# Kernel optimization log

Hardware: AMD Instinct MI355X
Metric: run time of the kernel (lower is better)

The kernel has to match this reference:

```python
import jax, jax.numpy as jnp
import numpy as np

NUM_HEADS = 4
LN_EPS = 1e-5


def layer_norm(x, g, b):
    mu = jnp.mean(x, axis=-1, keepdims=True)
    var = jnp.mean(jnp.square(x - mu), axis=-1, keepdims=True)
    return (x - mu) * jax.lax.rsqrt(var + LN_EPS) * g + b


def setup_inputs() -> dict:
    key = jax.random.key(0)
    ks = jax.random.split(key, 18)
    N, E, D = 40000, 640000, 128
    H = 4 * D  # MLP hidden
    s = 0.02
    inp = {
        'node_features': jax.random.normal(ks[0], (N, D), jnp.float32),
        'edge_index': jax.random.randint(ks[1], (2, E), 0, N, jnp.int64),
        'Wq': jax.random.normal(ks[2], (D, D), jnp.float32) * s,
        'bq': jnp.zeros((D,), jnp.float32),
        'Wk': jax.random.normal(ks[3], (D, D), jnp.float32) * s,
        'bk': jnp.zeros((D,), jnp.float32),
        'Wv': jax.random.normal(ks[4], (D, D), jnp.float32) * s,
        'bv': jnp.zeros((D,), jnp.float32),
        'Wo': jax.random.normal(ks[5], (D, D), jnp.float32) * s,
        'bo': jnp.zeros((D,), jnp.float32),
        'ln_g': jnp.ones((D,), jnp.float32),
        'ln_b': jnp.zeros((D,), jnp.float32),
        'W1': jax.random.normal(ks[6], (D, H), jnp.float32) * s,
        'b1': jnp.zeros((H,), jnp.float32),
        'W2': jax.random.normal(ks[7], (H, D), jnp.float32) * s,
        'b2': jnp.zeros((D,), jnp.float32),
    }
    return inp


def reference(node_features, edge_index, Wq, bq, Wk, bk, Wv, bv, Wo, bo,
              ln_g, ln_b, W1, b1, W2, b2):
    N, D = node_features.shape
    Hh = NUM_HEADS
    hd = D // Hh
    residual = node_features

    q = (node_features @ Wq + bq).reshape(N, Hh, hd)
    k = (node_features @ Wk + bk).reshape(N, Hh, hd)
    v = (node_features @ Wv + bv).reshape(N, Hh, hd)

    src, dst = edge_index[0], edge_index[1]
    # per-edge attention scores: [E, Hh]
    scores = jnp.einsum('ehd,ehd->eh', q[dst], k[src]) * (hd ** -0.5)

    # segment softmax over edges grouped by destination node
    seg_max = jax.ops.segment_max(scores, dst, num_segments=N)  # [N, Hh]
    seg_max = jnp.where(jnp.isfinite(seg_max), seg_max, 0.0)
    ex = jnp.exp(scores - seg_max[dst])
    seg_sum = jax.ops.segment_sum(ex, dst, num_segments=N)  # [N, Hh]
    w = ex / seg_sum[dst]  # [E, Hh]

    messages = w[:, :, None] * v[src]  # [E, Hh, hd]
    aggregated = jax.ops.segment_sum(messages, dst, num_segments=N)  # [N, Hh, hd]
    aggregated = aggregated.reshape(N, D)

    out = aggregated @ Wo + bo
    out = layer_norm(out + residual, ln_g, ln_b)
    mlp = jax.nn.gelu(out @ W1 + b1) @ W2 + b2
    return out + mlp
```

## Files before the change

kernel.cpp:

```cpp
#include <hip/hip_runtime.h>
#include <math.h>

#define D   128
#define HH  4
#define HD  32
#define HID 512
#define WPB 4
#define MT  32
#define XP  136
#define HHP 264
#define KVB 264
#define SCB 1024

typedef __attribute__((ext_vector_type(8))) short bf16x8;
typedef __attribute__((ext_vector_type(4))) float f32x4;
typedef __attribute__((ext_vector_type(2))) float f32x2;

__device__ __forceinline__ short f2b(float f) {
    unsigned u = __float_as_uint(f);
    unsigned r = (u + 0x7FFFu + ((u >> 16) & 1u)) >> 16;
    return (short)r;
}
__device__ __forceinline__ unsigned char f2fp8(float f) {
    return (unsigned char)(__builtin_amdgcn_cvt_pk_fp8_f32(f, f, 0, false) & 0xFF);
}

__device__ __forceinline__ float gelu_tanh(float x) {
    float u = 0.7978845608028654f * (x + 0.044715f * x * x * x);
    float e = __expf(2.0f * u);
    return x * e * __builtin_amdgcn_rcpf(e + 1.0f);
}

__global__ void k0_zero_deg(int* __restrict__ deg, int N) {
    int i = blockIdx.x * blockDim.x + threadIdx.x;
    if (i < N) deg[i] = 0;
}

__global__ void k_prep(const float* __restrict__ W1, const float* __restrict__ W2,
                       const float* __restrict__ Wq, const float* __restrict__ Wk,
                       const float* __restrict__ Wv, const float* __restrict__ Wo,
                       short* __restrict__ Wt1, short* __restrict__ Wt2,
                       short* __restrict__ Wtq, short* __restrict__ Wtk,
                       short* __restrict__ Wtv, short* __restrict__ Wto) {
    int i = blockIdx.x * 256 + threadIdx.x;
    {   int n = i >> 7, k = i & 127; Wt1[i] = f2b(W1[k * HID + n]); }
    {   int n = i >> 9, k = i & 511; Wt2[i] = f2b(W2[k * D + n]); }
    if (i < D * D) {
        int n = i >> 7, k = i & 127;
        Wtq[i] = f2b(Wq[k * D + n]);
        Wtk[i] = f2b(Wk[k * D + n]);
        Wtv[i] = f2b(Wv[k * D + n]);
        Wto[i] = f2b(Wo[k * D + n]);
    }
}

__global__ __launch_bounds__(256) void k1_qkv_mfma(
        const float* __restrict__ x,
        const short* __restrict__ Wtq, const float* __restrict__ bq,
        const short* __restrict__ Wtk, const float* __restrict__ bk,
        const short* __restrict__ Wtv, const float* __restrict__ bv,
        float* __restrict__ q, unsigned char* __restrict__ kv, int N) {
    __shared__ short xs[MT * XP];
    __shared__ unsigned char kvs[MT * KVB];
    int m0 = blockIdx.x * MT;
    int t = threadIdx.x;
    int wave = t >> 6, lane = t & 63, quad = lane >> 4, l16 = lane & 15;

    {
        int row = t >> 3, c0 = (t & 7) * 16;
        int n = m0 + row;
        #pragma unroll
        for (int c = 0; c < 16; c += 4) {
            float4 xv = {0.f, 0.f, 0.f, 0.f};
            if (n < N) xv = *(const float4*)(x + (size_t)n * D + c0 + c);
            xs[row * XP + c0 + c + 0] = f2b(xv.x);
            xs[row * XP + c0 + c + 1] = f2b(xv.y);
            xs[row * XP + c0 + c + 2] = f2b(xv.z);
            xs[row * XP + c0 + c + 3] = f2b(xv.w);
        }
    }
    __syncthreads();

    f32x4 accq[2][2], acck[2][2], accv[2][2];
    #pragma unroll
    for (int nt = 0; nt < 2; ++nt) {
        int c = wave * 32 + nt * 16 + l16;
        float q0 = bq[c], k0 = bk[c], v0 = bv[c];
        #pragma unroll
        for (int mt = 0; mt < 2; ++mt) {
            accq[mt][nt] = (f32x4){q0, q0, q0, q0};
            acck[mt][nt] = (f32x4){k0, k0, k0, k0};
            accv[mt][nt] = (f32x4){v0, v0, v0, v0};
        }
    }
    #pragma unroll
    for (int kt = 0; kt < 4; ++kt) {
        int klane = kt * 32 + quad * 8;
        bf16x8 a0 = *(const bf16x8*)(xs + (l16)      * XP + klane);
        bf16x8 a1 = *(const bf16x8*)(xs + (16 + l16) * XP + klane);
        #pragma unroll
        for (int nt = 0; nt < 2; ++nt) {
            int c = wave * 32 + nt * 16 + l16;
            bf16x8 fq = *(const bf16x8*)(Wtq + (size_t)c * D + klane);
            bf16x8 fk = *(const bf16x8*)(Wtk + (size_t)c * D + klane);
            bf16x8 fv = *(const bf16x8*)(Wtv + (size_t)c * D + klane);
            accq[0][nt] = __builtin_amdgcn_mfma_f32_16x16x32_bf16(a0, fq, accq[0][nt], 0, 0, 0);
            accq[1][nt] = __builtin_amdgcn_mfma_f32_16x16x32_bf16(a1, fq, accq[1][nt], 0, 0, 0);
            acck[0][nt] = __builtin_amdgcn_mfma_f32_16x16x32_bf16(a0, fk, acck[0][nt], 0, 0, 0);
            acck[1][nt] = __builtin_amdgcn_mfma_f32_16x16x32_bf16(a1, fk, acck[1][nt], 0, 0, 0);
            accv[0][nt] = __builtin_amdgcn_mfma_f32_16x16x32_bf16(a0, fv, accv[0][nt], 0, 0, 0);
            accv[1][nt] = __builtin_amdgcn_mfma_f32_16x16x32_bf16(a1, fv, accv[1][nt], 0, 0, 0);
        }
    }
    #pragma unroll
    for (int mt = 0; mt < 2; ++mt)
        #pragma unroll
        for (int nt = 0; nt < 2; ++nt)
            #pragma unroll
            for (int r = 0; r < 4; ++r) {
                int row = mt * 16 + quad * 4 + r;
                int n = m0 + row;
                int c = wave * 32 + nt * 16 + l16;
                if (n < N) q[(size_t)n * D + c] = accq[mt][nt][r];
                int base = row * KVB + (c >> 1) * 4 + (c & 1);
                kvs[base]     = f2fp8(acck[mt][nt][r]);
                kvs[base + 2] = f2fp8(accv[mt][nt][r]);
            }
    __syncthreads();
    {
        int row = t >> 3, c0 = (t & 7) * 32;
        int n = m0 + row;
        if (n < N) {
            *(uint4*)(kv + (size_t)n * 256 + c0) =
                *(const uint4*)(kvs + row * KVB + c0);
            *(uint4*)(kv + (size_t)n * 256 + c0 + 16) =
                *(const uint4*)(kvs + row * KVB + c0 + 16);
        }
    }
}

__global__ void k_hist(const int* __restrict__ dst, int* __restrict__ deg, int E) {
    int i = blockIdx.x * blockDim.x + threadIdx.x;
    if (i < E) atomicAdd(&deg[dst[i]], 1);
}

__global__ void k_scan1(const int* __restrict__ deg, int* __restrict__ partial, int N) {
    __shared__ int red[256];
    int b = blockIdx.x, t = threadIdx.x;
    int base = b * SCB + t * 4;
    int s = 0;
    #pragma unroll
    for (int i = 0; i < 4; ++i) { int idx = base + i; if (idx < N) s += deg[idx]; }
    red[t] = s;
    __syncthreads();
    for (int off = 128; off > 0; off >>= 1) {
        if (t < off) red[t] += red[t + off];
        __syncthreads();
    }
    if (t == 0) partial[b] = red[0];
}

__global__ void k_scan2(int* __restrict__ partial, int nb) {
    __shared__ int s[256];
    int t = threadIdx.x;
    int v0 = (t < nb) ? partial[t] : 0;
    s[t] = v0;
    __syncthreads();
    for (int off = 1; off < 256; off <<= 1) {
        int v = (t >= off) ? s[t - off] : 0;
        __syncthreads();
        s[t] += v;
        __syncthreads();
    }
    if (t < nb) partial[t] = s[t] - v0;
    if (t == nb - 1) partial[nb] = s[t];
}

__global__ void k_scan3(const int* __restrict__ deg, const int* __restrict__ partial,
                        int* __restrict__ row_ptr, int* __restrict__ cursor,
                        int N, int nb) {
    __shared__ int red[256];
    int b = blockIdx.x, t = threadIdx.x;
    int base = b * SCB + t * 4;
    int d0[4]; int s = 0;
    #pragma unroll
    for (int i = 0; i < 4; ++i) {
        int idx = base + i;
        d0[i] = (idx < N) ? deg[idx] : 0;
        s += d0[i];
    }
    red[t] = s;
    __syncthreads();
    for (int off = 1; off < 256; off <<= 1) {
        int v = (t >= off) ? red[t - off] : 0;
        __syncthreads();
        red[t] += v;
        __syncthreads();
    }
    int off0 = partial[b] + red[t] - s;
    #pragma unroll
    for (int i = 0; i < 4; ++i) {
        int idx = base + i;
        if (idx < N) { row_ptr[idx] = off0; cursor[idx] = off0; off0 += d0[i]; }
    }
    if (b == 0 && t == 0) row_ptr[N] = partial[nb];
}

__global__ void k_scatter(const int* __restrict__ src, const int* __restrict__ dst,
                          int* __restrict__ cursor, int* __restrict__ col, int E) {
    int i = blockIdx.x * blockDim.x + threadIdx.x;
    if (i < E) {
        int d = dst[i];
        int pos = atomicAdd(&cursor[d], 1);
        col[pos] = src[i];
    }
}

__global__ void k_attn(const float* __restrict__ q, const unsigned char* __restrict__ kv,
                       const int* __restrict__ row_ptr, const int* __restrict__ col,
                       float* __restrict__ agg, int N) {
    int wave = threadIdx.x >> 6;
    int lane = threadIdx.x & 63;
    int n = blockIdx.x * WPB + wave;
    if (n >= N) return;
    int beg = row_ptr[n], end = row_ptr[n + 1];

    float2 qv = *(const float2*)(q + (size_t)n * D + 2 * lane);

    float l = 0.f;
    float2 acc = {0.f, 0.f};

    unsigned pk_cur = 0;
    int sB = 0;
    if (beg < end) {
        int sA = col[beg];
        pk_cur = *(const unsigned*)(kv + (size_t)sA * 256 + 4 * lane);
    }
    if (beg + 1 < end) sB = col[beg + 1];

    for (int p = beg; p < end; ++p) {
        unsigned pk = pk_cur;
        int sC = (p + 2 < end) ? col[p + 2] : 0;
        if (p + 1 < end)
            pk_cur = *(const unsigned*)(kv + (size_t)sB * 256 + 4 * lane);
        sB = sC;

        f32x2 kp = __builtin_amdgcn_cvt_pk_f32_fp8((int)pk, false);
        f32x2 vp = __builtin_amdgcn_cvt_pk_f32_fp8((int)pk, true);
        float part = qv.x * kp.x + qv.y * kp.y;
        part += __shfl_xor(part, 1);
        part += __shfl_xor(part, 2);
        part += __shfl_xor(part, 4);
        part += __shfl_xor(part, 8);
        float pe = __expf(part * 0.17677669529663687f);
        l += pe;
        acc.x = fmaf(pe, vp.x, acc.x);
        acc.y = fmaf(pe, vp.y, acc.y);
    }
    float inv = (l > 0.f) ? 1.f / l : 0.f;
    float2 o = {acc.x * inv, acc.y * inv};
    *(float2*)(agg + (size_t)n * D + 2 * lane) = o;
}

__global__ __launch_bounds__(256) void k56_wo_ln_mlp(
        const float* __restrict__ agg, const short* __restrict__ Wto,
        const float* __restrict__ bo, const float* __restrict__ x,
        const float* __restrict__ g, const float* __restrict__ b,
        const short* __restrict__ Wt1, const float* __restrict__ b1,
        const short* __restrict__ Wt2, const float* __restrict__ b2,
        float* __restrict__ out, int N) {
    __shared__ short xs[MT * XP];
    __shared__ short hid[MT * HHP];
    __shared__ float ps[MT * 4], ps2[MT * 4];
    int m0 = blockIdx.x * MT;
    int t = threadIdx.x;
    int wave = t >> 6, lane = t & 63, quad = lane >> 4, l16 = lane & 15;

    {
        int row = t >> 3, c0 = (t & 7) * 16;
        int n = m0 + row;
        #pragma unroll
        for (int c = 0; c < 16; c += 4) {
            float4 xv = {0.f, 0.f, 0.f, 0.f};
            if (n < N) xv = *(const float4*)(agg + (size_t)n * D + c0 + c);
            xs[row * XP + c0 + c + 0] = f2b(xv.x);
            xs[row * XP + c0 + c + 1] = f2b(xv.y);
            xs[row * XP + c0 + c + 2] = f2b(xv.z);
            xs[row * XP + c0 + c + 3] = f2b(xv.w);
        }
    }
    __syncthreads();

    f32x4 acc[2][2];
    #pragma unroll
    for (int nt = 0; nt < 2; ++nt) {
        float bb = bo[wave * 32 + nt * 16 + l16];
        acc[0][nt] = (f32x4){bb, bb, bb, bb};
        acc[1][nt] = (f32x4){bb, bb, bb, bb};
    }
    #pragma unroll
    for (int kt = 0; kt < 4; ++kt) {
        int klane = kt * 32 + quad * 8;
        bf16x8 a0 = *(const bf16x8*)(xs + (l16)      * XP + klane);
        bf16x8 a1 = *(const bf16x8*)(xs + (16 + l16) * XP + klane);
        #pragma unroll
        for (int nt = 0; nt < 2; ++nt) {
            bf16x8 bf = *(const bf16x8*)(Wto + (size_t)(wave * 32 + nt * 16 + l16) * D + klane);
            acc[0][nt] = __builtin_amdgcn_mfma_f32_16x16x32_bf16(a0, bf, acc[0][nt], 0, 0, 0);
            acc[1][nt] = __builtin_amdgcn_mfma_f32_16x16x32_bf16(a1, bf, acc[1][nt], 0, 0, 0);
        }
    }
    float lnval[2][2][4];
    #pragma unroll
    for (int mt = 0; mt < 2; ++mt)
        #pragma unroll
        for (int nt = 0; nt < 2; ++nt)
            #pragma unroll
            for (int r = 0; r < 4; ++r) {
                int n = m0 + mt * 16 + quad * 4 + r;
                int c = wave * 32 + nt * 16 + l16;
                float v = acc[mt][nt][r];
                if (n < N) v += x[(size_t)n * D + c];
                lnval[mt][nt][r] = v;
            }

    #pragma unroll
    for (int mt = 0; mt < 2; ++mt)
        #pragma unroll
        for (int r = 0; r < 4; ++r) {
            float a0 = lnval[mt][0][r], a1 = lnval[mt][1][r];
            float s1 = a0 + a1;
            float s2 = a0 * a0 + a1 * a1;
            #pragma unroll
            for (int m = 1; m <= 8; m <<= 1) {
                s1 += __shfl_xor(s1, m);
                s2 += __shfl_xor(s2, m);
            }
            if (l16 == 0) {
                int row = mt * 16 + quad * 4 + r;
                ps[row * 4 + wave] = s1;
                ps2[row * 4 + wave] = s2;
            }
        }
    __syncthreads();

    #pragma unroll
    for (int mt = 0; mt < 2; ++mt)
        #pragma unroll
        for (int r = 0; r < 4; ++r) {
            int row = mt * 16 + quad * 4 + r;
            float4 p1 = *(const float4*)(ps + row * 4);
            float4 p2 = *(const float4*)(ps2 + row * 4);
            float mm = (p1.x + p1.y + p1.z + p1.w) * (1.0f / D);
            float m2 = (p2.x + p2.y + p2.z + p2.w) * (1.0f / D);
            float rs = rsqrtf(m2 - mm * mm + 1e-5f);
            #pragma unroll
            for (int nt = 0; nt < 2; ++nt) {
                int c = wave * 32 + nt * 16 + l16;
                float v = (lnval[mt][nt][r] - mm) * rs * g[c] + b[c];
                lnval[mt][nt][r] = v;
                xs[row * XP + c] = f2b(v);
            }
        }
    __syncthreads();

    f32x4 acc2[2][2];
    #pragma unroll
    for (int nt = 0; nt < 2; ++nt) {
        float bb = b2[wave * 32 + nt * 16 + l16];
        acc2[0][nt] = (f32x4){bb, bb, bb, bb};
        acc2[1][nt] = (f32x4){bb, bb, bb, bb};
    }
    #pragma unroll
    for (int h = 0; h < 2; ++h) {
        f32x4 acc1[2][4];
        #pragma unroll
        for (int nt = 0; nt < 4; ++nt) {
            float bb = b1[h * 256 + wave * 64 + nt * 16 + l16];
            acc1[0][nt] = (f32x4){bb, bb, bb, bb};
            acc1[1][nt] = (f32x4){bb, bb, bb, bb};
        }
        #pragma unroll
        for (int kt = 0; kt < 4; ++kt) {
            int klane = kt * 32 + quad * 8;
            bf16x8 a0 = *(const bf16x8*)(xs + (l16)      * XP + klane);
            bf16x8 a1 = *(const bf16x8*)(xs + (16 + l16) * XP + klane);
            #pragma unroll
            for (int nt = 0; nt < 4; ++nt) {
                int hc = h * 256 + wave * 64 + nt * 16 + l16;
                bf16x8 bf = *(const bf16x8*)(Wt1 + (size_t)hc * D + klane);
                acc1[0][nt] = __builtin_amdgcn_mfma_f32_16x16x32_bf16(a0, bf, acc1[0][nt], 0, 0, 0);
                acc1[1][nt] = __builtin_amdgcn_mfma_f32_16x16x32_bf16(a1, bf, acc1[1][nt], 0, 0, 0);
            }
        }
        __syncthreads();
        #pragma unroll
        for (int mt = 0; mt < 2; ++mt)
            #pragma unroll
            for (int nt = 0; nt < 4; ++nt)
                #pragma unroll
                for (int r = 0; r < 4; ++r) {
                    int row = mt * 16 + quad * 4 + r;
                    int lc = wave * 64 + nt * 16 + l16;
                    hid[row * HHP + lc] = f2b(gelu_tanh(acc1[mt][nt][r]));
                }
        __syncthreads();
        #pragma unroll
        for (int kt = 0; kt < 8; ++kt) {
            int klane = kt * 32 + quad * 8;
            bf16x8 a0 = *(const bf16x8*)(hid + (l16)      * HHP + klane);
            bf16x8 a1 = *(const bf16x8*)(hid + (16 + l16) * HHP + klane);
            #pragma unroll
            for (int nt = 0; nt < 2; ++nt) {
                bf16x8 bf = *(const bf16x8*)(Wt2 + (size_t)(wave * 32 + nt * 16 + l16) * HID
                                             + h * 256 + klane);
                acc2[0][nt] = __builtin_amdgcn_mfma_f32_16x16x32_bf16(a0, bf, acc2[0][nt], 0, 0, 0);
                acc2[1][nt] = __builtin_amdgcn_mfma_f32_16x16x32_bf16(a1, bf, acc2[1][nt], 0, 0, 0);
            }
        }
    }

    #pragma unroll
    for (int mt = 0; mt < 2; ++mt)
        #pragma unroll
        for (int nt = 0; nt < 2; ++nt)
            #pragma unroll
            for (int r = 0; r < 4; ++r) {
                int n = m0 + mt * 16 + quad * 4 + r;
                int c = wave * 32 + nt * 16 + l16;
                if (n < N)
                    out[(size_t)n * D + c] = lnval[mt][nt][r] + acc2[mt][nt][r];
            }
}

extern "C" void kernel_launch(void* const* d_in, const int* in_sizes, int n_in,
                              void* d_out, int out_size, void* d_ws, size_t ws_size,
                              hipStream_t stream) {
    const float* x   = (const float*)d_in[0];
    const int*   ei  = (const int*)d_in[1];
    const float* Wq  = (const float*)d_in[2];
    const float* bq  = (const float*)d_in[3];
    const float* Wk  = (const float*)d_in[4];
    const float* bk  = (const float*)d_in[5];
    const float* Wv  = (const float*)d_in[6];
    const float* bv  = (const float*)d_in[7];
    const float* Wo  = (const float*)d_in[8];
    const float* bo  = (const float*)d_in[9];
    const float* lng = (const float*)d_in[10];
    const float* lnb = (const float*)d_in[11];
    const float* W1  = (const float*)d_in[12];
    const float* b1  = (const float*)d_in[13];
    const float* W2  = (const float*)d_in[14];
    const float* b2  = (const float*)d_in[15];
    float* out = (float*)d_out;

    int N = in_sizes[0] / D;
    int E = in_sizes[1] / 2;
    const int* srcp = ei;
    const int* dstp = ei + E;

    short* Wt1 = (short*)d_ws;
    short* Wt2 = Wt1 + 512 * 128;
    short* Wtq = Wt2 + 512 * 128;
    short* Wtk = Wtq + 128 * 128;
    short* Wtv = Wtk + 128 * 128;
    short* Wto = Wtv + 128 * 128;
    float* q   = (float*)(Wto + 128 * 128);
    unsigned char* kv = (unsigned char*)(q + (size_t)N * D);
    float* agg = (float*)(kv + (size_t)N * 256);
    int*   deg     = (int*)(agg + (size_t)N * D);
    int*   row_ptr = deg + N;
    int*   cursor  = row_ptr + N + 1;
    int*   col     = cursor + N;
    int*   partial = col + E;

    int nblk32 = (N + MT - 1) / MT;
    int eblk   = (E + 255) / 256;
    int nbs    = (N + SCB - 1) / SCB;

    k0_zero_deg<<<(N + 255) / 256, 256, 0, stream>>>(deg, N);
    k_prep<<<(512 * 128) / 256, 256, 0, stream>>>(W1, W2, Wq, Wk, Wv, Wo,
                                                  Wt1, Wt2, Wtq, Wtk, Wtv, Wto);
    k_hist<<<eblk, 256, 0, stream>>>(dstp, deg, E);
    k1_qkv_mfma<<<nblk32, 256, 0, stream>>>(x, Wtq, bq, Wtk, bk, Wtv, bv, q, kv, N);
    k_scan1<<<nbs, 256, 0, stream>>>(deg, partial, N);
    k_scan2<<<1, 256, 0, stream>>>(partial, nbs);
    k_scan3<<<nbs, 256, 0, stream>>>(deg, partial, row_ptr, cursor, N, nbs);
    k_scatter<<<eblk, 256, 0, stream>>>(srcp, dstp, cursor, col, E);
    k_attn<<<(N + WPB - 1) / WPB, WPB * 64, 0, stream>>>(q, kv, row_ptr, col, agg, N);
    k56_wo_ln_mlp<<<nblk32, 256, 0, stream>>>(agg, Wto, bo, x, lng, lnb,
                                              Wt1, b1, Wt2, b2, out, N);
}
```

Before: 317.3 us.

## Process four edges per wave in attention with 16-byte packed K/V loads

The fp8 K/V interleave changes from 2-channel to 8-channel groups, so each lane can fetch 8 K and 8 V values in one 16-byte load. The attention kernel now splits each wave into four 16-lane groups, each handling a different incoming edge. This cuts the dot-product shuffle reduction to two steps and processes four edges per loop iteration. A cross-group shuffle reduction of the softmax sum and the 8 accumulators is added at the end. Padding iterations for degrees not divisible by four waste some lanes and use a validity mask.

```diff
diff --git a/kernel.cpp b/kernel.cpp
--- a/kernel.cpp
+++ b/kernel.cpp
@@ -122,9 +122,9 @@
                 int n = m0 + row;
                 int c = wave * 32 + nt * 16 + l16;
                 if (n < N) q[(size_t)n * D + c] = accq[mt][nt][r];
-                int base = row * KVB + (c >> 1) * 4 + (c & 1);
+                int base = row * KVB + 16 * (c >> 3) + (c & 7);
                 kvs[base]     = f2fp8(acck[mt][nt][r]);
-                kvs[base + 2] = f2fp8(accv[mt][nt][r]);
+                kvs[base + 8] = f2fp8(accv[mt][nt][r]);
             }
     __syncthreads();
     {
@@ -221,45 +221,70 @@
                        float* __restrict__ agg, int N) {
     int wave = threadIdx.x >> 6;
     int lane = threadIdx.x & 63;
+    int g = lane >> 4, s = lane & 15;
     int n = blockIdx.x * WPB + wave;
     if (n >= N) return;
     int beg = row_ptr[n], end = row_ptr[n + 1];
 
-    float2 qv = *(const float2*)(q + (size_t)n * D + 2 * lane);
-
+    float4 qa = *(const float4*)(q + (size_t)n * D + 8 * s);
+    float4 qb = *(const float4*)(q + (size_t)n * D + 8 * s + 4);
+
+    float acc[8] = {0.f, 0.f, 0.f, 0.f, 0.f, 0.f, 0.f, 0.f};
     float l = 0.f;
-    float2 acc = {0.f, 0.f};
-
-    unsigned pk_cur = 0;
-    int sB = 0;
-    if (beg < end) {
-        int sA = col[beg];
-        pk_cur = *(const unsigned*)(kv + (size_t)sA * 256 + 4 * lane);
-    }
-    if (beg + 1 < end) sB = col[beg + 1];
-
-    for (int p = beg; p < end; ++p) {
-        unsigned pk = pk_cur;
-        int sC = (p + 2 < end) ? col[p + 2] : 0;
-        if (p + 1 < end)
-            pk_cur = *(const unsigned*)(kv + (size_t)sB * 256 + 4 * lane);
-        sB = sC;
-
-        f32x2 kp = __builtin_amdgcn_cvt_pk_f32_fp8((int)pk, false);
-        f32x2 vp = __builtin_amdgcn_cvt_pk_f32_fp8((int)pk, true);
-        float part = qv.x * kp.x + qv.y * kp.y;
-        part += __shfl_xor(part, 1);
-        part += __shfl_xor(part, 2);
-        part += __shfl_xor(part, 4);
-        part += __shfl_xor(part, 8);
-        float pe = __expf(part * 0.17677669529663687f);
+
+    int np = (end - beg + 3) >> 2;
+    uint4 pk_cur = {0, 0, 0, 0};
+    int idx_next = 0;
+    if (np > 0) {
+        int c0 = col[min(beg + g, end - 1)];
+        pk_cur = *(const uint4*)(kv + (size_t)c0 * 256 + 16 * s);
+        if (np > 1) idx_next = col[min(beg + 4 + g, end - 1)];
+    }
+    for (int it = 0; it < np; ++it) {
+        uint4 pk = pk_cur;
+        bool valid = (beg + it * 4 + g) < end;
+        if (it + 1 < np) {
+            pk_cur = *(const uint4*)(kv + (size_t)idx_next * 256 + 16 * s);
+            if (it + 2 < np)
+                idx_next = col[min(beg + (it + 2) * 4 + g, end - 1)];
+        }
+        f32x2 k01 = __builtin_amdgcn_cvt_pk_f32_fp8((int)pk.x, false);
+        f32x2 k23 = __builtin_amdgcn_cvt_pk_f32_fp8((int)pk.x, true);
+        f32x2 k45 = __builtin_amdgcn_cvt_pk_f32_fp8((int)pk.y, false);
+        f32x2 k67 = __builtin_amdgcn_cvt_pk_f32_fp8((int)pk.y, true);
+        f32x2 v01 = __builtin_amdgcn_cvt_pk_f32_fp8((int)pk.z, false);
+        f32x2 v23 = __builtin_amdgcn_cvt_pk_f32_fp8((int)pk.z, true);
+        f32x2 v45 = __builtin_amdgcn_cvt_pk_f32_fp8((int)pk.w, false);
+        f32x2 v67 = __builtin_amdgcn_cvt_pk_f32_fp8((int)pk.w, true);
+        float d = qa.x * k01.x + qa.y * k01.y + qa.z * k23.x + qa.w * k23.y
+                + qb.x * k45.x + qb.y * k45.y + qb.z * k67.x + qb.w * k67.y;
+        d += __shfl_xor(d, 1);
+        d += __shfl_xor(d, 2);
+        float pe = __expf(d * 0.17677669529663687f);
+        pe = valid ? pe : 0.f;
         l += pe;
-        acc.x = fmaf(pe, vp.x, acc.x);
-        acc.y = fmaf(pe, vp.y, acc.y);
-    }
-    float inv = (l > 0.f) ? 1.f / l : 0.f;
-    float2 o = {acc.x * inv, acc.y * inv};
-    *(float2*)(agg + (size_t)n * D + 2 * lane) = o;
+        acc[0] = fmaf(pe, v01.x, acc[0]);
+        acc[1] = fmaf(pe, v01.y, acc[1]);
+        acc[2] = fmaf(pe, v23.x, acc[2]);
+        acc[3] = fmaf(pe, v23.y, acc[3]);
+        acc[4] = fmaf(pe, v45.x, acc[4]);
+        acc[5] = fmaf(pe, v45.y, acc[5]);
+        acc[6] = fmaf(pe, v67.x, acc[6]);
+        acc[7] = fmaf(pe, v67.y, acc[7]);
+    }
+    #pragma unroll
+    for (int m = 16; m <= 32; m <<= 1) {
+        l += __shfl_xor(l, m);
+        #pragma unroll
+        for (int i = 0; i < 8; ++i) acc[i] += __shfl_xor(acc[i], m);
+    }
+    if (g == 0) {
+        float inv = (l > 0.f) ? 1.f / l : 0.f;
+        float4 o1 = {acc[0] * inv, acc[1] * inv, acc[2] * inv, acc[3] * inv};
+        float4 o2 = {acc[4] * inv, acc[5] * inv, acc[6] * inv, acc[7] * inv};
+        *(float4*)(agg + (size_t)n * D + 8 * s)     = o1;
+        *(float4*)(agg + (size_t)n * D + 8 * s + 4) = o2;
+    }
 }
 
 __global__ __launch_bounds__(256) void k56_wo_ln_mlp(
```

New measurement: 277.4 us. -12.6%, faster.
